# Optimization experiments

Hardware: AMD Instinct MI355X
Metric: run time of the kernel (lower is better)

The kernel has to match this reference:

```python
import jax, jax.numpy as jnp
import numpy as np


def setup_inputs() -> dict:
    key = jax.random.key(0)
    k1, k2, k3, k4 = jax.random.split(key, 4)
    B, T, C, D = 4, 2048, 1024, 128
    x = jax.random.normal(k1, (B, T, C), dtype=jnp.float32)
    # torch nn.Linear(in, out, bias=False) computes x @ W.T with W [out,in];
    # we store W as [in,out] so projection is x @ W (same math, transposed layout).
    Wq = jax.random.normal(k2, (C, D), dtype=jnp.float32) * (C ** -0.5)
    Wk = jax.random.normal(k3, (C, D), dtype=jnp.float32) * (C ** -0.5)
    Wv = jax.random.normal(k4, (C, D), dtype=jnp.float32) * (C ** -0.5)
    return {"x": x, "Wq": Wq, "Wk": Wk, "Wv": Wv}


def reference(x, Wq, Wk, Wv):
    B, T, C = x.shape
    D = Wq.shape[1]
    q = jnp.einsum("btc,cd->btd", x, Wq)
    k = jnp.einsum("btc,cd->btd", x, Wk)
    v = jnp.einsum("btc,cd->btd", x, Wv)
    scores = jnp.einsum("btd,bsd->bts", q, k) * (D ** -0.5)  # [B,T,T]
    causal = jnp.tril(jnp.ones((T, T), dtype=bool))
    scores = jnp.where(causal, scores, -jnp.inf)
    attn = jax.nn.softmax(scores, axis=-1)  # dropout_rate=0.0 -> identity
    return jnp.einsum("bts,bsd->btd", attn, v)
```

## Files before the change

kernel.cpp:

```cpp
#include <hip/hip_runtime.h>
#include <hip/hip_bf16.h>

typedef __attribute__((ext_vector_type(8))) short bf16x8;
typedef __attribute__((ext_vector_type(4))) short bf16x4;
typedef __attribute__((ext_vector_type(4))) float f32x4;

#define Tq 2048
#define Cq 1024
#define Dq 128

typedef const __attribute__((address_space(1))) void* gas_t;
typedef __attribute__((address_space(3))) void* las_t;

__device__ __forceinline__ short f2bf(float f) {
  unsigned u = __float_as_uint(f);
  u += 0x7fffu + ((u >> 16) & 1u);
  return (short)(u >> 16);
}

__global__ __launch_bounds__(256) void pack_w_kernel(const float* __restrict__ Wq_,
                                                     const float* __restrict__ Wk_,
                                                     const float* __restrict__ Wv_,
                                                     short* __restrict__ wt) {
  int tid = blockIdx.x * 256 + threadIdx.x;
  int y   = tid >> 14;
  int idx = tid & 16383;
  int kg  = idx >> 7;
  int n   = idx & 127;
  const float* W = (y == 0) ? Wq_ : (y == 1 ? Wk_ : Wv_);
  float scale = (y == 0) ? 0.08838834764831845f : 1.0f;
  bf16x8 o;
  #pragma unroll
  for (int j = 0; j < 8; ++j) o[j] = f2bf(W[(size_t)(kg * 8 + j) * Dq + n] * scale);
  *reinterpret_cast<bf16x8*>(wt + (size_t)y * 131072 + (size_t)n * 1024 + kg * 8) = o;
}

__global__ __launch_bounds__(128) void qkv_gemm_kernel(const float* __restrict__ x,
                                                       const short* __restrict__ wt,
                                                       short* __restrict__ qb,
                                                       short* __restrict__ kb2,
                                                       short* __restrict__ vt) {
  __shared__ float As[2][32][64];
  __shared__ short Bs[2][128][64];
  int y  = blockIdx.y;
  int bm = blockIdx.x;
  int w  = threadIdx.x >> 6, l = threadIdx.x & 63;
  int r  = l & 15, h = l >> 4;
  const short* wy = wt + (size_t)y * 131072;

  auto stage = [&](int t, int bi) {
    int k0 = t * 64;
    #pragma unroll
    for (int i = 0; i < 4; ++i) {
      int ia  = w * 4 + i;
      int row = ia * 4 + (l >> 4);
      int g   = l & 15;
      int sg  = (g & 8) | ((g & 7) ^ (row & 7));
      __builtin_amdgcn_global_load_lds(
          (gas_t)(x + (size_t)(bm * 32 + row) * Cq + k0 + sg * 4),
          (las_t)(&As[bi][ia * 4][0]), 16, 0, 0);
    }
    #pragma unroll
    for (int i = 0; i < 8; ++i) {
      int ib  = w * 8 + i;
      int row = ib * 8 + (l >> 3);
      int sc  = ((l & 7) ^ (row & 7)) * 8;
      __builtin_amdgcn_global_load_lds(
          (gas_t)(wy + (size_t)row * Cq + k0 + sc),
          (las_t)(&Bs[bi][ib * 8][0]), 16, 0, 0);
    }
  };

  f32x4 acc[2][4] = {};
  stage(0, 0);
  int cur = 0;
  for (int t = 0; t < 16; ++t, cur ^= 1) {
    stage(t + 1 < 16 ? t + 1 : t, cur ^ 1);
    asm volatile("s_waitcnt vmcnt(12)" ::: "memory");
    __builtin_amdgcn_s_barrier();
    __builtin_amdgcn_sched_barrier(0);
    bf16x8 af[2][2], bf[4][2];
    #pragma unroll
    for (int mi = 0; mi < 2; ++mi)
      #pragma unroll
      for (int kt = 0; kt < 2; ++kt) {
        int row = mi * 16 + r;
        int g0  = kt * 8 + h * 2;
        int s0  = (g0 & 8) | ((g0 & 7) ^ (row & 7));
        int g1  = g0 + 1;
        int s1  = (g1 & 8) | ((g1 & 7) ^ (row & 7));
        f32x4 fa = *reinterpret_cast<const f32x4*>(&As[cur][row][s0 * 4]);
        f32x4 fb = *reinterpret_cast<const f32x4*>(&As[cur][row][s1 * 4]);
        union { bf16x8 v; unsigned u[4]; } cv;
        asm("v_cvt_pk_bf16_f32 %0, %1, %2" : "=v"(cv.u[0]) : "v"(fa[0]), "v"(fa[1]));
        asm("v_cvt_pk_bf16_f32 %0, %1, %2" : "=v"(cv.u[1]) : "v"(fa[2]), "v"(fa[3]));
        asm("v_cvt_pk_bf16_f32 %0, %1, %2" : "=v"(cv.u[2]) : "v"(fb[0]), "v"(fb[1]));
        asm("v_cvt_pk_bf16_f32 %0, %1, %2" : "=v"(cv.u[3]) : "v"(fb[2]), "v"(fb[3]));
        af[mi][kt] = cv.v;
      }
    #pragma unroll
    for (int ni = 0; ni < 4; ++ni)
      #pragma unroll
      for (int kt = 0; kt < 2; ++kt) {
        int row = w * 64 + ni * 16 + r;
        bf[ni][kt] = *reinterpret_cast<const bf16x8*>(
            &Bs[cur][row][(kt * 32 + h * 8) ^ ((row & 7) << 3)]);
      }
    #pragma unroll
    for (int kt = 0; kt < 2; ++kt)
      #pragma unroll
      for (int mi = 0; mi < 2; ++mi)
        #pragma unroll
        for (int ni = 0; ni < 4; ++ni)
          acc[mi][ni] = __builtin_amdgcn_mfma_f32_16x16x32_bf16(af[mi][kt], bf[ni][kt], acc[mi][ni], 0, 0, 0);
    __builtin_amdgcn_sched_barrier(0);
    __builtin_amdgcn_s_barrier();
  }

  #pragma unroll
  for (int mi = 0; mi < 2; ++mi) {
    #pragma unroll
    for (int ni = 0; ni < 4; ++ni) {
      #pragma unroll
      for (int reg = 0; reg < 4; ++reg) {
        int m = bm * 32 + mi * 16 + h * 4 + reg;
        int n = w * 64 + ni * 16 + r;
        short s = f2bf(acc[mi][ni][reg]);
        if (y == 0)      qb[(size_t)m * Dq + n] = s;
        else if (y == 1) kb2[(size_t)m * Dq + n] = s;
        else {
          int bb = m >> 11, t2 = m & 2047;
          vt[((size_t)bb * Dq + n) * Tq + t2] = s;
        }
      }
    }
  }
}

__global__ __launch_bounds__(256, 4) void attn_kernel(const short* __restrict__ qb,
                                                      const short* __restrict__ kb2,
                                                      const short* __restrict__ vtb,
                                                      float* __restrict__ pacc,
                                                      float* __restrict__ pml) {
  __shared__ struct {
    short kb[2][32][128];
    short vb[2][128][32];
    short pb[4][16][40];
  } sm;

  int bid = blockIdx.x;
  int b   = bid / 272;
  int s0i = bid - b * 272;
  int qi  = 31, off = 0;
  while (s0i >= off + ((qi >> 1) + 1)) { off += (qi >> 1) + 1; --qi; }
  int c   = s0i - off;
  int tid = threadIdx.x;
  int w   = tid >> 6, l = tid & 63;
  int r   = l & 15, h = l >> 4;

  int qw = qi * 64 + w * 16;
  const short* kbB = kb2 + (size_t)b * Tq * Dq;
  const short* vtB = vtb + (size_t)b * Dq * Tq;

  bf16x8 aq[4];
  size_t qbase = ((size_t)b * Tq + qw + r) * Dq;
  #pragma unroll
  for (int kt = 0; kt < 4; ++kt)
    aq[kt] = *reinterpret_cast<const bf16x8*>(qb + qbase + kt * 32 + h * 8);

  int ntall = 2 * qi + 2;
  int tbeg  = c * 4;
  int tend  = ntall < tbeg + 4 ? ntall : tbeg + 4;

  f32x4 acc[8] = {};
  float mrun = -1e30f, lrun = 0.0f;

  {
    auto stage = [&](int it, int bi) {
      int kv0 = it * 32;
      #pragma unroll
      for (int i2 = 0; i2 < 2; ++i2) {
        int i = w * 2 + i2;
        int row = i * 4 + (l >> 4);
        int sc  = ((l & 15) * 8) ^ ((row & 7) << 3);
        __builtin_amdgcn_global_load_lds(
            (gas_t)(kbB + (size_t)(kv0 + row) * Dq + sc),
            (las_t)(&sm.kb[bi][i * 4][0]), 16, 0, 0);
      }
      #pragma unroll
      for (int i2 = 0; i2 < 2; ++i2) {
        int i = w * 2 + i2;
        int row = i * 16 + (l >> 2);
        int sc  = ((l & 3) * 8) ^ ((row & 3) << 3);
        __builtin_amdgcn_global_load_lds(
            (gas_t)(vtB + (size_t)row * Tq + kv0 + sc),
            (las_t)(&sm.vb[bi][i * 16][0]), 16, 0, 0);
      }
    };

    stage(tbeg, 0);
    int cur = 0;
    for (int t = tbeg; t < tend; ++t, cur ^= 1) {
      stage(t + 1 < tend ? t + 1 : t, cur ^ 1);
      asm volatile("s_waitcnt vmcnt(4)" ::: "memory");
      __builtin_amdgcn_s_barrier();
      __builtin_amdgcn_sched_barrier(0);

      int kv0 = t * 32;
      bf16x8 kf[8];
      #pragma unroll
      for (int nt = 0; nt < 2; ++nt)
        #pragma unroll
        for (int kt = 0; kt < 4; ++kt) {
          int row = nt * 16 + r;
          kf[nt * 4 + kt] = *reinterpret_cast<const bf16x8*>(
              &sm.kb[cur][row][(kt * 32 + h * 8) ^ ((row & 7) << 3)]);
        }
      f32x4 s[2] = {};
      #pragma unroll
      for (int nt = 0; nt < 2; ++nt)
        #pragma unroll
        for (int kt = 0; kt < 4; ++kt)
          s[nt] = __builtin_amdgcn_mfma_f32_16x16x32_bf16(
              kf[nt * 4 + kt], aq[kt], s[nt], 0, 0, 0);

      bf16x8 vf[8];
      #pragma unroll
      for (int dt = 0; dt < 8; ++dt) {
        int row = dt * 16 + r;
        vf[dt] = *reinterpret_cast<const bf16x8*>(
            &sm.vb[cur][row][(h * 8) ^ ((row & 3) << 3)]);
      }

      if (kv0 + 31 > qw) {
        #pragma unroll
        for (int nt = 0; nt < 2; ++nt)
          #pragma unroll
          for (int reg = 0; reg < 4; ++reg)
            if (kv0 + nt * 16 + h * 4 + reg > qw + r) s[nt][reg] = -1e30f;
      }

      float mx = fmaxf(fmaxf(fmaxf(s[0][0], s[0][1]), fmaxf(s[0][2], s[0][3])),
                       fmaxf(fmaxf(s[1][0], s[1][1]), fmaxf(s[1][2], s[1][3])));
      mx = fmaxf(mx, __shfl_xor(mx, 16));
      mx = fmaxf(mx, __shfl_xor(mx, 32));
      float mnew  = fmaxf(mrun, mx);
      float alpha = __expf(mrun - mnew);
      mrun = mnew;
      float p[2][4];
      #pragma unroll
      for (int nt = 0; nt < 2; ++nt)
        #pragma unroll
        for (int reg = 0; reg < 4; ++reg)
          p[nt][reg] = s[nt][reg] > -1e29f ? __expf(s[nt][reg] - mnew) : 0.0f;
      float rsum = ((p[0][0] + p[0][1]) + (p[0][2] + p[0][3])) +
                   ((p[1][0] + p[1][1]) + (p[1][2] + p[1][3]));
      rsum += __shfl_xor(rsum, 16);
      rsum += __shfl_xor(rsum, 32);
      lrun = lrun * alpha + rsum;

      float af[4];
      #pragma unroll
      for (int reg = 0; reg < 4; ++reg) af[reg] = __shfl(alpha, h * 4 + reg);
      #pragma unroll
      for (int dt = 0; dt < 8; ++dt)
        #pragma unroll
        for (int reg = 0; reg < 4; ++reg) acc[dt][reg] *= af[reg];

      #pragma unroll
      for (int nt = 0; nt < 2; ++nt) {
        bf16x4 w4;
        #pragma unroll
        for (int reg = 0; reg < 4; ++reg) w4[reg] = f2bf(p[nt][reg]);
        *reinterpret_cast<bf16x4*>(&sm.pb[w][r][nt * 16 + h * 4]) = w4;
      }
      asm volatile("s_waitcnt lgkmcnt(0)" ::: "memory");
      __builtin_amdgcn_sched_barrier(0);
      bf16x8 ap = *reinterpret_cast<const bf16x8*>(&sm.pb[w][r][h * 8]);

      #pragma unroll
      for (int dt = 0; dt < 8; ++dt)
        acc[dt] = __builtin_amdgcn_mfma_f32_16x16x32_bf16(ap, vf[dt], acc[dt], 0, 0, 0);

      __builtin_amdgcn_sched_barrier(0);
      __builtin_amdgcn_s_barrier();
    }
  }

  if (h == 0) {
    pml[((size_t)bid * 64 + w * 16 + r) * 2 + 0] = mrun;
    pml[((size_t)bid * 64 + w * 16 + r) * 2 + 1] = lrun;
  }
  #pragma unroll
  for (int dt = 0; dt < 8; ++dt)
    #pragma unroll
    for (int reg = 0; reg < 4; ++reg) {
      int row = w * 16 + h * 4 + reg;
      pacc[((size_t)bid * 64 + row) * 128 + dt * 16 + r] = acc[dt][reg];
    }
}

__global__ __launch_bounds__(256) void combine_kernel(const float* __restrict__ pacc,
                                                      const float* __restrict__ pml,
                                                      float* __restrict__ out) {
  int gid = blockIdx.x * 256 + threadIdx.x;
  int rg  = gid >> 5;
  int c4  = (gid & 31) * 4;
  int b      = rg >> 11;
  int rowInB = rg & 2047;
  int qi     = rowInB >> 6;
  int row    = rowInB & 63;
  int m    = qi >> 1;
  int F    = (qi & 1) ? (m + 1) * (m + 2) : (m + 1) * (m + 1);
  int base = b * 272 + 272 - F;
  int nch  = m + 1;

  float Ms = -1e30f;
  for (int cc = 0; cc < nch; ++cc)
    Ms = fmaxf(Ms, pml[((size_t)(base + cc) * 64 + row) * 2 + 0]);
  float den = 0.0f;
  f32x4 num = {};
  for (int cc = 0; cc < nch; ++cc) {
    float M = pml[((size_t)(base + cc) * 64 + row) * 2 + 0];
    float L = pml[((size_t)(base + cc) * 64 + row) * 2 + 1];
    float e = __expf(M - Ms);
    den += e * L;
    f32x4 a = *reinterpret_cast<const f32x4*>(
        pacc + ((size_t)(base + cc) * 64 + row) * 128 + c4);
    num += a * e;
  }
  f32x4 o = num * (1.0f / den);
  *reinterpret_cast<f32x4*>(out + ((size_t)b * Tq + qi * 64 + row) * Dq + c4) = o;
}

extern "C" void kernel_launch(void* const* d_in, const int* in_sizes, int n_in,
                              void* d_out, int out_size, void* d_ws, size_t ws_size,
                              hipStream_t stream) {
  const float* x   = (const float*)d_in[0];
  const float* Wq_ = (const float*)d_in[1];
  const float* Wk_ = (const float*)d_in[2];
  const float* Wv_ = (const float*)d_in[3];
  float* out = (float*)d_out;
  char* ws = (char*)d_ws;
  short* wt   = (short*)(ws);
  short* qb   = (short*)(ws + 786432);
  short* kb   = (short*)(ws + 2883584);
  short* vt   = (short*)(ws + 4980736);
  float* pml  = (float*)(ws + 7077888);
  float* pacc = (float*)(ws + 7634944);

  hipLaunchKernelGGL(pack_w_kernel, dim3(192), dim3(256), 0, stream, Wq_, Wk_, Wv_, wt);
  hipLaunchKernelGGL(qkv_gemm_kernel, dim3(256, 3), dim3(128), 0, stream, x, wt, qb, kb, vt);
  hipLaunchKernelGGL(attn_kernel, dim3(1088), dim3(256), 0, stream, qb, kb, vt, pacc, pml);
  hipLaunchKernelGGL(combine_kernel, dim3(1024), dim3(256), 0, stream, pacc, pml, out);
}
```

Measured before the change: 61.35 us.

## Rebalance split-KV chunks, lazy softmax rescale, bf16 partial accumulators

Changes the split-KV partition from fixed 4-tile chunks (272 blocks per batch) to a balanced split of each query tile's KV range into nch_of(qi) nearly equal chunks, giving exactly 256 blocks per batch. Adds a lazy online-softmax rescale that skips the alpha multiply when the new max exceeds the running max by at most 8, which removes per-iteration shuffles and multiplies. Stores the partial accumulators as bf16 instead of fp32 to halve the traffic between the attention and combine kernels, and adds a sched_barrier between the K fragment loads and the MFMAs. The cost is lower precision in the partial sums, a wave-uniform branch, and possible exp overflow margin with the lazy max.

```diff
diff --git a/kernel.cpp b/kernel.cpp
--- a/kernel.cpp
+++ b/kernel.cpp
@@ -16,6 +16,12 @@
   unsigned u = __float_as_uint(f);
   u += 0x7fffu + ((u >> 16) & 1u);
   return (short)(u >> 16);
+}
+__device__ __forceinline__ float bf2f(short s) {
+  return __uint_as_float(((unsigned)(unsigned short)s) << 16);
+}
+__device__ __forceinline__ int nch_of(int qi) {
+  return (2 * qi + 6) / 5 + 1;
 }
 
 __global__ __launch_bounds__(256) void pack_w_kernel(const float* __restrict__ Wq_,
@@ -140,7 +146,7 @@
 __global__ __launch_bounds__(256, 4) void attn_kernel(const short* __restrict__ qb,
                                                       const short* __restrict__ kb2,
                                                       const short* __restrict__ vtb,
-                                                      float* __restrict__ pacc,
+                                                      short* __restrict__ pacc,
                                                       float* __restrict__ pml) {
   __shared__ struct {
     short kb[2][32][128];
@@ -149,11 +155,16 @@
   } sm;
 
   int bid = blockIdx.x;
-  int b   = bid / 272;
-  int s0i = bid - b * 272;
+  int b   = bid >> 8;
+  int s0i = bid & 255;
   int qi  = 31, off = 0;
-  while (s0i >= off + ((qi >> 1) + 1)) { off += (qi >> 1) + 1; --qi; }
-  int c   = s0i - off;
+  for (;;) {
+    int n = nch_of(qi);
+    if (s0i < off + n) break;
+    off += n; --qi;
+  }
+  int c    = s0i - off;
+  int nch  = nch_of(qi);
   int tid = threadIdx.x;
   int w   = tid >> 6, l = tid & 63;
   int r   = l & 15, h = l >> 4;
@@ -169,8 +180,8 @@
     aq[kt] = *reinterpret_cast<const bf16x8*>(qb + qbase + kt * 32 + h * 8);
 
   int ntall = 2 * qi + 2;
-  int tbeg  = c * 4;
-  int tend  = ntall < tbeg + 4 ? ntall : tbeg + 4;
+  int tbeg  = (c * ntall) / nch;
+  int tend  = ((c + 1) * ntall) / nch;
 
   f32x4 acc[8] = {};
   float mrun = -1e30f, lrun = 0.0f;
@@ -216,6 +227,7 @@
           kf[nt * 4 + kt] = *reinterpret_cast<const bf16x8*>(
               &sm.kb[cur][row][(kt * 32 + h * 8) ^ ((row & 7) << 3)]);
         }
+      __builtin_amdgcn_sched_barrier(0);
       f32x4 s[2] = {};
       #pragma unroll
       for (int nt = 0; nt < 2; ++nt)
@@ -244,28 +256,32 @@
                        fmaxf(fmaxf(s[1][0], s[1][1]), fmaxf(s[1][2], s[1][3])));
       mx = fmaxf(mx, __shfl_xor(mx, 16));
       mx = fmaxf(mx, __shfl_xor(mx, 32));
-      float mnew  = fmaxf(mrun, mx);
-      float alpha = __expf(mrun - mnew);
-      mrun = mnew;
+
+      float lmul = 1.0f;
+      if (!__all(mx - mrun <= 8.0f)) {
+        float mnew  = fmaxf(mrun, mx);
+        float alpha = __expf(mrun - mnew);
+        mrun = mnew;
+        lmul = alpha;
+        float af[4];
+        #pragma unroll
+        for (int reg = 0; reg < 4; ++reg) af[reg] = __shfl(alpha, h * 4 + reg);
+        #pragma unroll
+        for (int dt = 0; dt < 8; ++dt)
+          #pragma unroll
+          for (int reg = 0; reg < 4; ++reg) acc[dt][reg] *= af[reg];
+      }
       float p[2][4];
       #pragma unroll
       for (int nt = 0; nt < 2; ++nt)
         #pragma unroll
         for (int reg = 0; reg < 4; ++reg)
-          p[nt][reg] = s[nt][reg] > -1e29f ? __expf(s[nt][reg] - mnew) : 0.0f;
+          p[nt][reg] = s[nt][reg] > -1e29f ? __expf(s[nt][reg] - mrun) : 0.0f;
       float rsum = ((p[0][0] + p[0][1]) + (p[0][2] + p[0][3])) +
                    ((p[1][0] + p[1][1]) + (p[1][2] + p[1][3]));
       rsum += __shfl_xor(rsum, 16);
       rsum += __shfl_xor(rsum, 32);
-      lrun = lrun * alpha + rsum;
-
-      float af[4];
-      #pragma unroll
-      for (int reg = 0; reg < 4; ++reg) af[reg] = __shfl(alpha, h * 4 + reg);
-      #pragma unroll
-      for (int dt = 0; dt < 8; ++dt)
-        #pragma unroll
-        for (int reg = 0; reg < 4; ++reg) acc[dt][reg] *= af[reg];
+      lrun = lrun * lmul + rsum;
 
       #pragma unroll
       for (int nt = 0; nt < 2; ++nt) {
@@ -296,11 +312,11 @@
     #pragma unroll
     for (int reg = 0; reg < 4; ++reg) {
       int row = w * 16 + h * 4 + reg;
-      pacc[((size_t)bid * 64 + row) * 128 + dt * 16 + r] = acc[dt][reg];
-    }
-}
-
-__global__ __launch_bounds__(256) void combine_kernel(const float* __restrict__ pacc,
+      pacc[((size_t)bid * 64 + row) * 128 + dt * 16 + r] = f2bf(acc[dt][reg]);
+    }
+}
+
+__global__ __launch_bounds__(256) void combine_kernel(const short* __restrict__ pacc,
                                                       const float* __restrict__ pml,
                                                       float* __restrict__ out) {
   int gid = blockIdx.x * 256 + threadIdx.x;
@@ -310,10 +326,9 @@
   int rowInB = rg & 2047;
   int qi     = rowInB >> 6;
   int row    = rowInB & 63;
-  int m    = qi >> 1;
-  int F    = (qi & 1) ? (m + 1) * (m + 2) : (m + 1) * (m + 1);
-  int base = b * 272 + 272 - F;
-  int nch  = m + 1;
+  int base = b * 256;
+  for (int q2 = 31; q2 > qi; --q2) base += nch_of(q2);
+  int nch = nch_of(qi);
 
   float Ms = -1e30f;
   for (int cc = 0; cc < nch; ++cc)
@@ -325,9 +340,10 @@
     float L = pml[((size_t)(base + cc) * 64 + row) * 2 + 1];
     float e = __expf(M - Ms);
     den += e * L;
-    f32x4 a = *reinterpret_cast<const f32x4*>(
+    bf16x4 a = *reinterpret_cast<const bf16x4*>(
         pacc + ((size_t)(base + cc) * 64 + row) * 128 + c4);
-    num += a * e;
+    #pragma unroll
+    for (int j = 0; j < 4; ++j) num[j] += bf2f(a[j]) * e;
   }
   f32x4 o = num * (1.0f / den);
   *reinterpret_cast<f32x4*>(out + ((size_t)b * Tq + qi * 64 + row) * Dq + c4) = o;
@@ -347,10 +363,10 @@
   short* kb   = (short*)(ws + 2883584);
   short* vt   = (short*)(ws + 4980736);
   float* pml  = (float*)(ws + 7077888);
-  float* pacc = (float*)(ws + 7634944);
+  short* pacc = (short*)(ws + 7602176);
 
   hipLaunchKernelGGL(pack_w_kernel, dim3(192), dim3(256), 0, stream, Wq_, Wk_, Wv_, wt);
   hipLaunchKernelGGL(qkv_gemm_kernel, dim3(256, 3), dim3(128), 0, stream, x, wt, qb, kb, vt);
-  hipLaunchKernelGGL(attn_kernel, dim3(1088), dim3(256), 0, stream, qb, kb, vt, pacc, pml);
+  hipLaunchKernelGGL(attn_kernel, dim3(1024), dim3(256), 0, stream, qb, kb, vt, pacc, pml);
   hipLaunchKernelGGL(combine_kernel, dim3(1024), dim3(256), 0, stream, pacc, pml, out);
 }
```

Result: faster. 59.03 us (-3.8%).
